# Kernel optimization log

Measured on AMD Instinct MI355X. Metric: run time of the kernel, lower is better.

Reference implementation:

```python
import jax, jax.numpy as jnp
import numpy as np

B, S, D = 8, 512, 1024
F = 4 * D        # FFN hidden
E = 8            # num experts
SCALE = 0.02


def setup_inputs() -> dict:
    key = jax.random.key(0)
    ks = jax.random.split(key, 16)
    n = lambda k, shape, s=SCALE: (jax.random.normal(k, shape, dtype=jnp.float32) * s)
    task_ids = jax.random.randint(ks[15], (B,), 0, E)
    return {
        "hidden_states": jax.random.normal(ks[0], (B, S, D), dtype=jnp.float32),
        "ohe_task": jax.nn.one_hot(task_ids, E, dtype=jnp.float32),
        # base model (2-layer FFN) params
        "W1": n(ks[1], (D, F)), "b1": n(ks[2], (F,)),
        "W2": n(ks[3], (F, D)), "b2": n(ks[4], (D,)),
        # expert task vectors (expert_sd - base_sd), stacked over experts
        "T_W1": n(ks[5], (E, D, F)), "T_b1": n(ks[6], (E, F)),
        "T_W2": n(ks[7], (E, F, D)), "T_b2": n(ks[8], (E, D)),
        # gate: 2 hidden ReLU layers then linear to E
        "Wg1": n(ks[9], (D, D)), "bg1": jnp.zeros((D,), jnp.float32),
        "Wg2": n(ks[10], (D, D)), "bg2": jnp.zeros((D,), jnp.float32),
        "Wgo": n(ks[11], (D, E)), "bgo": jnp.zeros((E,), jnp.float32),
    }


def reference(hidden_states, ohe_task, W1, b1, W2, b2,
              T_W1, T_b1, T_W2, T_b2,
              Wg1, bg1, Wg2, bg2, Wgo, bgo):
    x = hidden_states  # [B,S,D]
    # --- router: per-token logits -> softmax over experts -> mean over seq ---
    h = jax.nn.relu(jnp.einsum("bsd,de->bse", x, Wg1) + bg1)
    h = jax.nn.relu(jnp.einsum("bsd,de->bse", h, Wg2) + bg2)
    logits = jnp.einsum("bsd,de->bse", h, Wgo) + bgo        # [B,S,E]
    gate_weights = jax.nn.softmax(logits, axis=-1).mean(axis=1)  # [B,E]
    # --- per-sample weighted merge of expert task vectors into base params ---
    coeff = gate_weights + ohe_task                          # [B,E]
    W1b = W1 + jnp.einsum("be,edf->bdf", coeff, T_W1)        # [B,D,F]
    b1b = b1 + coeff @ T_b1                                  # [B,F]
    W2b = W2 + jnp.einsum("be,efd->bfd", coeff, T_W2)        # [B,F,D]
    b2b = b2 + coeff @ T_b2                                  # [B,D]
    # --- batched functional forward through merged FFN ---
    hmid = jax.nn.gelu(jnp.einsum("bsd,bdf->bsf", x, W1b) + b1b[:, None, :],
                       approximate=False)
    out = jnp.einsum("bsf,bfd->bsd", hmid, W2b) + b2b[:, None, :]
    return out, gate_weights
```

## Files before the change

kernel.cpp:

```cpp
#include <hip/hip_runtime.h>
#include <hip/hip_bf16.h>

typedef __attribute__((ext_vector_type(8))) short s16x8;
typedef __attribute__((ext_vector_type(4))) float f32x4;

#define GLOAD_LDS16(gsrc, ldst) \
  __builtin_amdgcn_global_load_lds((const __attribute__((address_space(1))) void*)(gsrc), \
      (__attribute__((address_space(3))) void*)(ldst), 16, 0, 0)

__global__ __launch_bounds__(256) void cvt_bf16(const float* __restrict__ in,
                                                __hip_bfloat16* __restrict__ out, long n) {
  long i = ((long)blockIdx.x * 256 + threadIdx.x) * 4;
  if (i + 3 >= n) return;
  float4 v = *(const float4*)(in + i);
  __hip_bfloat16 tmp[4] = {__float2bfloat16(v.x), __float2bfloat16(v.y),
                           __float2bfloat16(v.z), __float2bfloat16(v.w)};
  *(ushort4*)((unsigned short*)out + i) = *(const ushort4*)tmp;
}

template<int NB>
__global__ __launch_bounds__(256) void merge_transpose(
    const float* __restrict__ Wb, const float* __restrict__ T,
    const float* __restrict__ coeff, __hip_bfloat16* __restrict__ Out,
    int K, int N, int nE) {
  int ntn = N >> 6;
  int k0 = (blockIdx.x / ntn) << 6;
  int n0 = (blockIdx.x % ntn) << 6;
  int t = threadIdx.x;
  long KN = (long)K * N;

  float4 accb[NB][4];
#pragma unroll
  for (int i = 0; i < 4; ++i) {
    int e = i * 256 + t; int kk = e >> 4, nn = (e & 15) << 2;
    float4 bv = *(const float4*)&Wb[(long)(k0 + kk) * N + n0 + nn];
#pragma unroll
    for (int b2 = 0; b2 < NB; ++b2) accb[b2][i] = bv;
  }
  for (int ex = 0; ex < nE; ++ex) {
    float c[NB];
#pragma unroll
    for (int b2 = 0; b2 < NB; ++b2) c[b2] = coeff[b2 * 8 + ex];
#pragma unroll
    for (int i = 0; i < 4; ++i) {
      int e = i * 256 + t; int kk = e >> 4, nn = (e & 15) << 2;
      float4 tv = *(const float4*)&T[(long)ex * KN + (long)(k0 + kk) * N + n0 + nn];
#pragma unroll
      for (int b2 = 0; b2 < NB; ++b2) {
        accb[b2][i].x += c[b2] * tv.x; accb[b2][i].y += c[b2] * tv.y;
        accb[b2][i].z += c[b2] * tv.z; accb[b2][i].w += c[b2] * tv.w;
      }
    }
  }
  __shared__ __hip_bfloat16 lds[64 * 66];
  for (int b2 = 0; b2 < NB; ++b2) {
    __syncthreads();
#pragma unroll
    for (int i = 0; i < 4; ++i) {
      int e = i * 256 + t; int kk = e >> 4, nn = (e & 15) << 2;
      lds[kk * 66 + nn + 0] = __float2bfloat16(accb[b2][i].x);
      lds[kk * 66 + nn + 1] = __float2bfloat16(accb[b2][i].y);
      lds[kk * 66 + nn + 2] = __float2bfloat16(accb[b2][i].z);
      lds[kk * 66 + nn + 3] = __float2bfloat16(accb[b2][i].w);
    }
    __syncthreads();
#pragma unroll
    for (int i = 0; i < 4; ++i) {
      int o = i * 256 + t; int n2 = o >> 4, k2 = (o & 15) << 2;
      __hip_bfloat16 tmp[4];
#pragma unroll
      for (int j = 0; j < 4; ++j) tmp[j] = lds[(k2 + j) * 66 + n2];
      *(ushort4*)((unsigned short*)&Out[(long)b2 * KN + (long)(n0 + n2) * K + k0 + k2]) =
          *(const ushort4*)tmp;
    }
  }
}

__global__ __launch_bounds__(256) void merge_bias(const float* __restrict__ base,
                                                  const float* __restrict__ T,
                                                  const float* __restrict__ coeff,
                                                  float* __restrict__ out, int n) {
  int b = blockIdx.y;
  int i = blockIdx.x * 256 + threadIdx.x;
  if (i >= n) return;
  float v = base[i];
#pragma unroll
  for (int e = 0; e < 8; ++e) v += coeff[b * 8 + e] * T[(long)e * n + i];
  out[(long)b * n + i] = v;
}

template<int MODE, int ACT, bool OUTBF>
__global__ __launch_bounds__(256, 2) void gemm_bt(
    const __hip_bfloat16* __restrict__ A, const __hip_bfloat16* __restrict__ BT,
    const float* __restrict__ bias, void* __restrict__ Out,
    int N, int K, long sA, long sB, long sBias, long sOut,
    int kLen, long ksOut) {
  int bid = blockIdx.x;
  int b, m, n, kc = 0;
  if (MODE == 0)      { b = blockIdx.y; m = (bid & 7) * 4 + ((bid >> 3) & 3); n = bid >> 5; }
  else                { b = bid & 7; int tile = bid >> 3; m = tile & 3; n = (tile >> 2) & 7; kc = tile >> 5; }
  int m0 = m << 7, n0 = n << 7;
  int kOff = kc * kLen;

  const __hip_bfloat16* Ab = A + (long)b * sA;
  const __hip_bfloat16* Bb = BT + (long)b * sB;

  __shared__ __align__(16) __hip_bfloat16 As[128 * 64];
  __shared__ __align__(16) __hip_bfloat16 Bs[128 * 64];

  int t = threadIdx.x;
  int lane = t & 63;
  int wid = t >> 6;
  int wm = wid >> 1, wn = wid & 1;
  int lr = lane & 15, kg = lane >> 4;

  f32x4 acc[4][4] = {};

  for (int kt = kOff; kt < kOff + kLen; kt += 64) {
#pragma unroll
    for (int is = 0; is < 4; ++is) {
      int ci = is * 256 + t;
      int row = ci >> 3, cpos = ci & 7;
      int csrc = cpos ^ (row & 7);
      GLOAD_LDS16(Ab + (long)(m0 + row) * K + kt + csrc * 8, &As[ci * 8]);
      GLOAD_LDS16(Bb + (long)(n0 + row) * K + kt + csrc * 8, &Bs[ci * 8]);
    }
    __syncthreads();
#pragma unroll
    for (int ks = 0; ks < 2; ++ks) {
      s16x8 af[4], bfr[4];
#pragma unroll
      for (int mi = 0; mi < 4; ++mi) {
        int row = wm * 64 + mi * 16 + lr;
        int c = (ks * 4 + kg) ^ (row & 7);
        af[mi] = *(const s16x8*)&As[row * 64 + c * 8];
      }
#pragma unroll
      for (int ni = 0; ni < 4; ++ni) {
        int row = wn * 64 + ni * 16 + lr;
        int c = (ks * 4 + kg) ^ (row & 7);
        bfr[ni] = *(const s16x8*)&Bs[row * 64 + c * 8];
      }
#pragma unroll
      for (int mi = 0; mi < 4; ++mi)
#pragma unroll
        for (int ni = 0; ni < 4; ++ni)
          acc[mi][ni] = __builtin_amdgcn_mfma_f32_16x16x32_bf16(bfr[ni], af[mi], acc[mi][ni], 0, 0, 0);
    }
    __syncthreads();
  }

#pragma unroll
  for (int mi = 0; mi < 4; ++mi) {
    int row = m0 + wm * 64 + mi * 16 + lr;
#pragma unroll
    for (int ni = 0; ni < 4; ++ni) {
      int colb = n0 + wn * 64 + ni * 16 + kg * 4;
      float bv4[4] = {0.f, 0.f, 0.f, 0.f};
      if (bias != nullptr) {
        float4 bb = *(const float4*)&bias[(long)b * sBias + colb];
        bv4[0] = bb.x; bv4[1] = bb.y; bv4[2] = bb.z; bv4[3] = bb.w;
      }
      float v[4];
#pragma unroll
      for (int j = 0; j < 4; ++j) {
        v[j] = acc[mi][ni][j] + bv4[j];
        if (ACT == 1) v[j] = fmaxf(v[j], 0.f);
        else if (ACT == 2) v[j] = 0.5f * v[j] * (1.f + erff(v[j] * 0.70710678118f));
      }
      long off = kc * ksOut + (long)b * sOut + (long)row * N + colb;
      if (OUTBF) {
        __hip_bfloat16 tmp[4] = {__float2bfloat16(v[0]), __float2bfloat16(v[1]),
                                 __float2bfloat16(v[2]), __float2bfloat16(v[3])};
        *(ushort4*)((unsigned short*)Out + off) = *(const ushort4*)tmp;
      } else {
        *(float4*)((float*)Out + off) = make_float4(v[0], v[1], v[2], v[3]);
      }
    }
  }
}

__global__ __launch_bounds__(512, 2) void gemm256_l1(
    const __hip_bfloat16* __restrict__ A, const __hip_bfloat16* __restrict__ BT,
    const float* __restrict__ bias, __hip_bfloat16* __restrict__ Out) {
  int bid = blockIdx.x;
  int b = bid & 7;
  int tile = bid >> 3;
  int m0 = (tile & 1) << 8;
  int n0 = (tile >> 1) << 8;
  const int K = 1024, N = 4096;

  const __hip_bfloat16* Ab = A + (long)b * 512 * 1024;
  const __hip_bfloat16* Bb = BT + (long)b * 4096 * 1024;
  const float* biasb = bias + (long)b * 4096;

  __shared__ __align__(16) __hip_bfloat16 As[2][256 * 64];
  __shared__ __align__(16) __hip_bfloat16 Bs[2][256 * 64];

  int t = threadIdx.x;
  int lane = t & 63;
  int wid = t >> 6;
  int wm = wid >> 2;
  int wn = wid & 3;
  int lr = lane & 15, kg = lane >> 4;

  f32x4 acc[8][4] = {};

  auto stage = [&](int buf, int kt) {
#pragma unroll
    for (int is = 0; is < 4; ++is) {
      int ci = is * 512 + t;
      int row = ci >> 3, cpos = ci & 7;
      int csrc = cpos ^ (row & 7);
      GLOAD_LDS16(Ab + (long)(m0 + row) * K + kt + csrc * 8, &As[buf][ci * 8]);
    }
#pragma unroll
    for (int is = 0; is < 4; ++is) {
      int ci = is * 512 + t;
      int row = ci >> 3, cpos = ci & 7;
      int csrc = cpos ^ (row & 7);
      GLOAD_LDS16(Bb + (long)(n0 + row) * K + kt + csrc * 8, &Bs[buf][ci * 8]);
    }
  };

  auto compute = [&](int buf) {
#pragma unroll
    for (int ks = 0; ks < 2; ++ks) {
      s16x8 af[8], bfr[4];
#pragma unroll
      for (int mi = 0; mi < 8; ++mi) {
        int row = wm * 128 + mi * 16 + lr;
        int c = (ks * 4 + kg) ^ (row & 7);
        af[mi] = *(const s16x8*)&As[buf][row * 64 + c * 8];
      }
#pragma unroll
      for (int ni = 0; ni < 4; ++ni) {
        int row = wn * 64 + ni * 16 + lr;
        int c = (ks * 4 + kg) ^ (row & 7);
        bfr[ni] = *(const s16x8*)&Bs[buf][row * 64 + c * 8];
      }
#pragma unroll
      for (int mi = 0; mi < 8; ++mi)
#pragma unroll
        for (int ni = 0; ni < 4; ++ni)
          acc[mi][ni] = __builtin_amdgcn_mfma_f32_16x16x32_bf16(bfr[ni], af[mi], acc[mi][ni], 0, 0, 0);
    }
  };

  const int nk = 16;
  stage(0, 0);
  for (int it = 0; it < nk; ++it) {
    if (it + 1 < nk) {
      stage((it + 1) & 1, (it + 1) << 6);
      asm volatile("s_waitcnt vmcnt(8)" ::: "memory");
    } else {
      asm volatile("s_waitcnt vmcnt(0)" ::: "memory");
    }
    asm volatile("s_barrier" ::: "memory");
    compute(it & 1);
    asm volatile("s_barrier" ::: "memory");
  }

#pragma unroll
  for (int mi = 0; mi < 8; ++mi) {
    int row = m0 + wm * 128 + mi * 16 + lr;
#pragma unroll
    for (int ni = 0; ni < 4; ++ni) {
      int colb = n0 + wn * 64 + ni * 16 + kg * 4;
      float4 bb = *(const float4*)&biasb[colb];
      float v[4] = {acc[mi][ni][0] + bb.x, acc[mi][ni][1] + bb.y,
                    acc[mi][ni][2] + bb.z, acc[mi][ni][3] + bb.w};
#pragma unroll
      for (int j = 0; j < 4; ++j)
        v[j] = 0.5f * v[j] * (1.f + erff(v[j] * 0.70710678118f));
      long off = (long)b * 512 * 4096 + (long)row * N + colb;
      __hip_bfloat16 tmp[4] = {__float2bfloat16(v[0]), __float2bfloat16(v[1]),
                               __float2bfloat16(v[2]), __float2bfloat16(v[3])};
      *(ushort4*)((unsigned short*)Out + off) = *(const ushort4*)tmp;
    }
  }
}

__global__ __launch_bounds__(256) void reduce2_bias(
    const __hip_bfloat16* __restrict__ p, const float* __restrict__ b2b,
    float* __restrict__ out, long ksOut) {
  long i = ((long)blockIdx.x * 256 + threadIdx.x) * 8;
  const unsigned short* ps = (const unsigned short*)p;
  ushort4 a0 = *(const ushort4*)(ps + i);
  ushort4 a1 = *(const ushort4*)(ps + i + 4);
  ushort4 c0 = *(const ushort4*)(ps + ksOut + i);
  ushort4 c1 = *(const ushort4*)(ps + ksOut + i + 4);
  int d = (int)(i & 1023);
  int b = (int)(i >> 19);
  const float* bp = b2b + (long)b * 1024 + d;
  float o[8];
  unsigned short av[8] = {a0.x, a0.y, a0.z, a0.w, a1.x, a1.y, a1.z, a1.w};
  unsigned short cv[8] = {c0.x, c0.y, c0.z, c0.w, c1.x, c1.y, c1.z, c1.w};
#pragma unroll
  for (int j = 0; j < 8; ++j) {
    __hip_bfloat16 ab = *(__hip_bfloat16*)&av[j], cb = *(__hip_bfloat16*)&cv[j];
    o[j] = __bfloat162float(ab) + __bfloat162float(cb) + bp[j];
  }
  *(float4*)(out + i) = make_float4(o[0], o[1], o[2], o[3]);
  *(float4*)(out + i + 4) = make_float4(o[4], o[5], o[6], o[7]);
}

__global__ __launch_bounds__(256) void router_logits(
    const __hip_bfloat16* __restrict__ Hg2, const float* __restrict__ Wgo,
    const float* __restrict__ bgo, float* __restrict__ probs) {
  int r = blockIdx.x;
  int t = threadIdx.x;
  float acc[8] = {};
#pragma unroll
  for (int j = 0; j < 4; ++j) {
    int k = j * 256 + t;
    float h = __bfloat162float(Hg2[(long)r * 1024 + k]);
    const float4* wp = (const float4*)&Wgo[k * 8];
    float4 w0 = wp[0], w1 = wp[1];
    acc[0] += h * w0.x; acc[1] += h * w0.y; acc[2] += h * w0.z; acc[3] += h * w0.w;
    acc[4] += h * w1.x; acc[5] += h * w1.y; acc[6] += h * w1.z; acc[7] += h * w1.w;
  }
#pragma unroll
  for (int off = 32; off >= 1; off >>= 1)
#pragma unroll
    for (int e = 0; e < 8; ++e) acc[e] += __shfl_down(acc[e], off);
  __shared__ float lds[4][8];
  int wid = t >> 6, lane = t & 63;
  if (lane == 0)
#pragma unroll
    for (int e = 0; e < 8; ++e) lds[wid][e] = acc[e];
  __syncthreads();
  if (t == 0) {
    float lg[8];
#pragma unroll
    for (int e = 0; e < 8; ++e) lg[e] = lds[0][e] + lds[1][e] + lds[2][e] + lds[3][e] + bgo[e];
    float mx = lg[0];
#pragma unroll
    for (int e = 1; e < 8; ++e) mx = fmaxf(mx, lg[e]);
    float s = 0.f;
#pragma unroll
    for (int e = 0; e < 8; ++e) { lg[e] = __expf(lg[e] - mx); s += lg[e]; }
    float inv = 1.f / s;
#pragma unroll
    for (int e = 0; e < 8; ++e) probs[(long)r * 8 + e] = lg[e] * inv;
  }
}

__global__ __launch_bounds__(256) void router_mean(
    const float* __restrict__ probs, const float* __restrict__ ohe,
    float* __restrict__ gate_out, float* __restrict__ coeff) {
  int b = blockIdx.x;
  int t = threadIdx.x;
  int e = t & 7, sg = t >> 3;
  float s = 0.f;
#pragma unroll
  for (int j = 0; j < 16; ++j)
    s += probs[((long)b * 512 + sg + j * 32) * 8 + e];
  __shared__ float lds[256];
  lds[t] = s;
  __syncthreads();
  if (t < 8) {
    float tot = 0.f;
#pragma unroll
    for (int g = 0; g < 32; ++g) tot += lds[g * 8 + t];
    float gw = tot / 512.f;
    gate_out[b * 8 + t] = gw;
    coeff[b * 8 + t] = gw + ohe[b * 8 + t];
  }
}

extern "C" void kernel_launch(void* const* d_in, const int* in_sizes, int n_in,
                              void* d_out, int out_size, void* d_ws, size_t ws_size,
                              hipStream_t stream) {
  const float* x    = (const float*)d_in[0];
  const float* ohe  = (const float*)d_in[1];
  const float* W1   = (const float*)d_in[2];
  const float* b1   = (const float*)d_in[3];
  const float* W2   = (const float*)d_in[4];
  const float* b2   = (const float*)d_in[5];
  const float* T_W1 = (const float*)d_in[6];
  const float* T_b1 = (const float*)d_in[7];
  const float* T_W2 = (const float*)d_in[8];
  const float* T_b2 = (const float*)d_in[9];
  const float* Wg1  = (const float*)d_in[10];
  const float* bg1  = (const float*)d_in[11];
  const float* Wg2  = (const float*)d_in[12];
  const float* bg2  = (const float*)d_in[13];
  const float* Wgo  = (const float*)d_in[14];
  const float* bgo  = (const float*)d_in[15];
  float* out = (float*)d_out;
  float* gate_out = out + (long)8 * 512 * 1024;

  char* w = (char*)d_ws;
  __hip_bfloat16* xb   = (__hip_bfloat16*)(w);
  __hip_bfloat16* Wg1T = (__hip_bfloat16*)(w + 8388608);
  __hip_bfloat16* Wg2T = (__hip_bfloat16*)(w + 10485760);
  __hip_bfloat16* Hg1  = (__hip_bfloat16*)(w + 12582912);
  __hip_bfloat16* Hg2  = (__hip_bfloat16*)(w + 20971520);
  float*          probs= (float*)(w + 29360128);
  float*          coeff= (float*)(w + 29491200);
  float*          b1b  = (float*)(w + 29492224);
  float*          b2b  = (float*)(w + 29623296);
  __hip_bfloat16* hmid = (__hip_bfloat16*)(w + 29656064);
  __hip_bfloat16* Wb   = (__hip_bfloat16*)(w + 63210496);
  __hip_bfloat16* part = (__hip_bfloat16*)(w);

  const long SSD = (long)512 * 1024;
  const long SSF = (long)512 * 4096;

  cvt_bf16<<<4096, 256, 0, stream>>>(x, xb, (long)8 * 512 * 1024);
  merge_transpose<1><<<16 * 16, 256, 0, stream>>>(Wg1, nullptr, nullptr, Wg1T, 1024, 1024, 0);
  merge_transpose<1><<<16 * 16, 256, 0, stream>>>(Wg2, nullptr, nullptr, Wg2T, 1024, 1024, 0);
  gemm_bt<0, 1, true><<<dim3(256, 1), 256, 0, stream>>>(xb, Wg1T, bg1, Hg1,
      1024, 1024, 0, 0, 0, 0, 1024, 0);
  gemm_bt<0, 1, true><<<dim3(256, 1), 256, 0, stream>>>(Hg1, Wg2T, bg2, Hg2,
      1024, 1024, 0, 0, 0, 0, 1024, 0);
  router_logits<<<4096, 256, 0, stream>>>(Hg2, Wgo, bgo, probs);
  router_mean<<<8, 256, 0, stream>>>(probs, ohe, gate_out, coeff);
  merge_bias<<<dim3(16, 8), 256, 0, stream>>>(b1, T_b1, coeff, b1b, 4096);
  merge_bias<<<dim3(4, 8), 256, 0, stream>>>(b2, T_b2, coeff, b2b, 1024);
  merge_transpose<8><<<16 * 64, 256, 0, stream>>>(W1, T_W1, coeff, Wb, 1024, 4096, 8);
  gemm256_l1<<<dim3(256, 1), 512, 0, stream>>>(xb, Wb, b1b, hmid);
  merge_transpose<8><<<64 * 16, 256, 0, stream>>>(W2, T_W2, coeff, Wb, 4096, 1024, 8);
  gemm_bt<2, 0, true><<<dim3(512, 1), 256, 0, stream>>>(hmid, Wb, nullptr, part,
      1024, 4096, SSF, (long)4096 * 1024, 0, SSD, 2048, (long)8 * 512 * 1024);
  reduce2_bias<<<2048, 256, 0, stream>>>(part, b2b, out, (long)8 * 512 * 1024);
}
```

Measured before the change: 271.9 us.

## Shrink layer-1 GEMM tile to 128x256 and drop LDS double buffering

The first FFN GEMM kernel changes from a 256x256 tile with double-buffered LDS and manual vmcnt pipelining to a 128x256 tile with a single LDS buffer and plain __syncthreads. The grid doubles to 512 blocks and launch bounds now request 4 blocks per SM instead of 2. The aim is more waves, better CU fill and fewer accumulator registers. In exchange it gives up overlap of global loads with MFMA inside a block and re-reads more of the B operand across tiles.

```diff
diff --git a/kernel.cpp b/kernel.cpp
--- a/kernel.cpp
+++ b/kernel.cpp
@@ -180,22 +180,22 @@
   }
 }
 
-__global__ __launch_bounds__(512, 2) void gemm256_l1(
+__global__ __launch_bounds__(512, 4) void gemm_l1(
     const __hip_bfloat16* __restrict__ A, const __hip_bfloat16* __restrict__ BT,
     const float* __restrict__ bias, __hip_bfloat16* __restrict__ Out) {
+  const int K = 1024, N = 4096;
   int bid = blockIdx.x;
   int b = bid & 7;
   int tile = bid >> 3;
-  int m0 = (tile & 1) << 8;
-  int n0 = (tile >> 1) << 8;
-  const int K = 1024, N = 4096;
+  int m0 = (tile & 3) << 7;
+  int n0 = (tile >> 2) << 8;
 
   const __hip_bfloat16* Ab = A + (long)b * 512 * 1024;
   const __hip_bfloat16* Bb = BT + (long)b * 4096 * 1024;
   const float* biasb = bias + (long)b * 4096;
 
-  __shared__ __align__(16) __hip_bfloat16 As[2][256 * 64];
-  __shared__ __align__(16) __hip_bfloat16 Bs[2][256 * 64];
+  __shared__ __align__(16) __hip_bfloat16 As[128 * 64];
+  __shared__ __align__(16) __hip_bfloat16 Bs[256 * 64];
 
   int t = threadIdx.x;
   int lane = t & 63;
@@ -204,66 +204,51 @@
   int wn = wid & 3;
   int lr = lane & 15, kg = lane >> 4;
 
-  f32x4 acc[8][4] = {};
-
-  auto stage = [&](int buf, int kt) {
+  f32x4 acc[4][4] = {};
+
+  for (int kt = 0; kt < K; kt += 64) {
+#pragma unroll
+    for (int is = 0; is < 2; ++is) {
+      int ci = is * 512 + t;
+      int row = ci >> 3, cpos = ci & 7;
+      int csrc = cpos ^ (row & 7);
+      GLOAD_LDS16(Ab + (long)(m0 + row) * K + kt + csrc * 8, &As[ci * 8]);
+    }
 #pragma unroll
     for (int is = 0; is < 4; ++is) {
       int ci = is * 512 + t;
       int row = ci >> 3, cpos = ci & 7;
       int csrc = cpos ^ (row & 7);
-      GLOAD_LDS16(Ab + (long)(m0 + row) * K + kt + csrc * 8, &As[buf][ci * 8]);
-    }
-#pragma unroll
-    for (int is = 0; is < 4; ++is) {
-      int ci = is * 512 + t;
-      int row = ci >> 3, cpos = ci & 7;
-      int csrc = cpos ^ (row & 7);
-      GLOAD_LDS16(Bb + (long)(n0 + row) * K + kt + csrc * 8, &Bs[buf][ci * 8]);
-    }
-  };
-
-  auto compute = [&](int buf) {
+      GLOAD_LDS16(Bb + (long)(n0 + row) * K + kt + csrc * 8, &Bs[ci * 8]);
+    }
+    __syncthreads();
 #pragma unroll
     for (int ks = 0; ks < 2; ++ks) {
-      s16x8 af[8], bfr[4];
-#pragma unroll
-      for (int mi = 0; mi < 8; ++mi) {
-        int row = wm * 128 + mi * 16 + lr;
+      s16x8 af[4], bfr[4];
+#pragma unroll
+      for (int mi = 0; mi < 4; ++mi) {
+        int row = wm * 64 + mi * 16 + lr;
         int c = (ks * 4 + kg) ^ (row & 7);
-        af[mi] = *(const s16x8*)&As[buf][row * 64 + c * 8];
+        af[mi] = *(const s16x8*)&As[row * 64 + c * 8];
       }
 #pragma unroll
       for (int ni = 0; ni < 4; ++ni) {
         int row = wn * 64 + ni * 16 + lr;
         int c = (ks * 4 + kg) ^ (row & 7);
-        bfr[ni] = *(const s16x8*)&Bs[buf][row * 64 + c * 8];
-      }
-#pragma unroll
-      for (int mi = 0; mi < 8; ++mi)
+        bfr[ni] = *(const s16x8*)&Bs[row * 64 + c * 8];
+      }
+#pragma unroll
+      for (int mi = 0; mi < 4; ++mi)
 #pragma unroll
         for (int ni = 0; ni < 4; ++ni)
           acc[mi][ni] = __builtin_amdgcn_mfma_f32_16x16x32_bf16(bfr[ni], af[mi], acc[mi][ni], 0, 0, 0);
     }
-  };
-
-  const int nk = 16;
-  stage(0, 0);
-  for (int it = 0; it < nk; ++it) {
-    if (it + 1 < nk) {
-      stage((it + 1) & 1, (it + 1) << 6);
-      asm volatile("s_waitcnt vmcnt(8)" ::: "memory");
-    } else {
-      asm volatile("s_waitcnt vmcnt(0)" ::: "memory");
-    }
-    asm volatile("s_barrier" ::: "memory");
-    compute(it & 1);
-    asm volatile("s_barrier" ::: "memory");
-  }
-
-#pragma unroll
-  for (int mi = 0; mi < 8; ++mi) {
-    int row = m0 + wm * 128 + mi * 16 + lr;
+    __syncthreads();
+  }
+
+#pragma unroll
+  for (int mi = 0; mi < 4; ++mi) {
+    int row = m0 + wm * 64 + mi * 16 + lr;
 #pragma unroll
     for (int ni = 0; ni < 4; ++ni) {
       int colb = n0 + wn * 64 + ni * 16 + kg * 4;
@@ -420,7 +405,7 @@
   merge_bias<<<dim3(16, 8), 256, 0, stream>>>(b1, T_b1, coeff, b1b, 4096);
   merge_bias<<<dim3(4, 8), 256, 0, stream>>>(b2, T_b2, coeff, b2b, 1024);
   merge_transpose<8><<<16 * 64, 256, 0, stream>>>(W1, T_W1, coeff, Wb, 1024, 4096, 8);
-  gemm256_l1<<<dim3(256, 1), 512, 0, stream>>>(xb, Wb, b1b, hmid);
+  gemm_l1<<<dim3(512, 1), 512, 0, stream>>>(xb, Wb, b1b, hmid);
   merge_transpose<8><<<64 * 16, 256, 0, stream>>>(W2, T_W2, coeff, Wb, 4096, 1024, 8);
   gemm_bt<2, 0, true><<<dim3(512, 1), 256, 0, stream>>>(hmid, Wb, nullptr, part,
       1024, 4096, SSF, (long)4096 * 1024, 0, SSD, 2048, (long)8 * 512 * 1024);
```

After: 258.6 us. 1.05x faster.
